# Performance work log

Measured on AMD Instinct MI355X. Metric: run time of the kernel, lower is better.

The kernel has to match this reference:

```python
import jax, jax.numpy as jnp
import numpy as np

L, B = 128, 64
IN_F, ACT_F, H = 512, 512, 1024
LSTM_IN = IN_F + ACT_F  # concat injection


def setup_inputs() -> dict:
    key = jax.random.key(0)
    ks = jax.random.split(key, 8)
    k = 1.0 / np.sqrt(H)  # torch LSTMCell init scale
    return {
        "input_feature": jax.random.normal(ks[0], (B, IN_F), dtype=jnp.float32),
        "action_features": jax.random.normal(ks[1], (L, B, ACT_F), dtype=jnp.float32),
        "hidden_state": jnp.zeros((B, H), dtype=jnp.float32),
        "state": jnp.zeros((B, H), dtype=jnp.float32),
        "W_ih": jax.random.uniform(ks[2], (4 * H, LSTM_IN), minval=-k, maxval=k, dtype=jnp.float32),
        "W_hh": jax.random.uniform(ks[3], (4 * H, H), minval=-k, maxval=k, dtype=jnp.float32),
        "b_ih": jax.random.uniform(ks[4], (4 * H,), minval=-k, maxval=k, dtype=jnp.float32),
        "b_hh": jax.random.uniform(ks[5], (4 * H,), minval=-k, maxval=k, dtype=jnp.float32),
    }


def reference(input_feature, action_features, hidden_state, state, W_ih, W_hh, b_ih, b_hh):
    # Per-timestep LSTMCell with concat injection of input_feature.
    # input_feature: [B, IN_F]; action_features: [L, B, ACT_F]
    def step(carry, a_t):
        h, c = carry
        x = jnp.concatenate([input_feature, a_t], axis=-1)  # inject_input (concat)
        gates = x @ W_ih.T + b_ih + h @ W_hh.T + b_hh  # [B, 4H]
        i, f, g, o = jnp.split(gates, 4, axis=-1)
        i = jax.nn.sigmoid(i)
        f = jax.nn.sigmoid(f)
        g = jnp.tanh(g)
        o = jax.nn.sigmoid(o)
        c1 = f * c + i * g
        h1 = o * jnp.tanh(c1)
        return (h1, c1), h1

    (h_n, c_n), hs = jax.lax.scan(step, (hidden_state, state), action_features)
    # hs: [L, B, H] stacked hidden states (PaddedSequenceWithMask.data)
    return hs, h_n, c_n
```

## Files before the change

kernel.cpp:

```cpp
#include <hip/hip_runtime.h>


#define LSTEPS 128
#define B 64
#define ACTF 512
#define H 1024
#define NB 128
#define HC 8
#define GSTR 37

typedef short s16x8 __attribute__((ext_vector_type(8)));
typedef short s16x4 __attribute__((ext_vector_type(4)));
typedef float f32x4 __attribute__((ext_vector_type(4)));
typedef unsigned short u16;
typedef unsigned long long u64;

__device__ __forceinline__ u16 f2bf(float f) {
  return __builtin_bit_cast(u16, (__bf16)f);
}
__device__ __forceinline__ float sigm(float x) { return 1.f / (1.f + __expf(-x)); }
__device__ __forceinline__ float tanh_fast(float x) { return 2.f / (1.f + __expf(-2.f * x)) - 1.f; }

__global__ void k_setup(const float* __restrict__ act, u16* __restrict__ actb,
                        const float* __restrict__ Wih, const float* __restrict__ Whh,
                        u16* __restrict__ wg,
                        const float* __restrict__ h0, u16* __restrict__ hbp,
                        const float* __restrict__ inf, const float* __restrict__ bih,
                        const float* __restrict__ bhh, float* __restrict__ pre0) {
  const int bb = blockIdx.x;
  const int tid = threadIdx.x;
  if (bb < 2048) {
    int id = bb * 256 + tid;
    const float4* s = (const float4*)act + (size_t)id * 2;
    float4 a = s[0], b = s[1];
    s16x8 o;
    o[0] = (short)f2bf(a.x); o[1] = (short)f2bf(a.y); o[2] = (short)f2bf(a.z); o[3] = (short)f2bf(a.w);
    o[4] = (short)f2bf(b.x); o[5] = (short)f2bf(b.y); o[6] = (short)f2bf(b.z); o[7] = (short)f2bf(b.w);
    int t = id >> 12, m = (id >> 6) & 63, ch = id & 63;
    ((s16x8*)actb)[t * 4096 + ch * 64 + m] = o;
  } else if (bb < 5120) {
    int idx = (bb - 2048) * 256 + tid;
    int bk = idx / 6144;
    int lin = idx - bk * 6144;
    int kt = lin >> 7, T = (lin >> 6) & 1, lane = lin & 63;
    int q = lane >> 4, r = lane & 15;
    int local = T * 16 + r;
    int j = (local >> 3) * 1024 + bk * 8 + (local & 7);
    int k = kt * 32 + q * 8;
    const float* src = (k < 512) ? (Wih + (size_t)j * 1024 + 512 + k)
                                 : (Whh + (size_t)j * 1024 + (k - 512));
    s16x8 o;
#pragma unroll
    for (int e = 0; e < 8; ++e) o[e] = (short)f2bf(src[e]);
    ((s16x8*)wg)[(size_t)bk * 6144 + lin] = o;
  } else if (bb < 5152) {
    int id = (bb - 5120) * 256 + tid;
    int blk2 = id >> 6, row = id & 63;
    const float* s = h0 + (size_t)row * H + blk2 * 8;
    s16x8 o;
#pragma unroll
    for (int e = 0; e < 8; ++e) o[e] = (short)f2bf(s[e]);
    o[0] = (short)((o[0] & ~1) | 1);
    ((s16x8*)(hbp + 65536))[blk2 * 64 + row] = o;
  } else if (bb < 5184) {
    int id = (bb - 5152) * 256 + tid;
    s16x8 p;
#pragma unroll
    for (int e = 0; e < 8; ++e) p[e] = 1;
    ((s16x8*)hbp)[id] = p;
  } else {
    int o = (bb - 5184) * 256 + tid;
    int bk = o >> 11;
    int rr = o & 2047;
    int b = rr >> 5;
    int local = rr & 31;
    int j = (local >> 3) * 1024 + bk * 8 + (local & 7);
    const float4* xa = (const float4*)(inf + (size_t)b * 512);
    const float4* wa = (const float4*)(Wih + (size_t)j * 1024);
    float s = 0.f;
#pragma unroll 4
    for (int k = 0; k < 128; ++k) {
      float4 x = xa[k], w = wa[k];
      s += x.x * w.x + x.y * w.y + x.z * w.z + x.w * w.w;
    }
    pre0[o] = s + bih[j] + bhh[j];
  }
}

#define AISS(dst, ptr) \
  asm volatile("global_load_dwordx4 %0, %1, off" : "=v"(dst) : "v"(ptr) : "memory");
#define HISS(dst, ptr) \
  asm volatile("global_load_dwordx4 %0, %1, off sc0 sc1" : "=v"(dst) : "v"(ptr) : "memory");
#define WAITV(N) { asm volatile("s_waitcnt vmcnt(" #N ")" ::: "memory"); \
                   __builtin_amdgcn_sched_barrier(0); }
#define LGKM0()  { asm volatile("s_waitcnt lgkmcnt(0)" ::: "memory"); }

__global__ void __launch_bounds__(256, 1) k_rnn(
    const u16* __restrict__ actb, const u16* __restrict__ wg,
    const float* __restrict__ pre0, const float* __restrict__ cinit,
    u16* __restrict__ hbp, unsigned* __restrict__ dump,
    float* __restrict__ out) {
  extern __shared__ char smem[];
  u16* wlds  = (u16*)smem;
  float* gl  = (float*)(smem + 98304);
  u16* hloc  = (u16*)(smem + 98304 + 37888);

  const int tid = threadIdx.x;
  const int bk = blockIdx.x;
  const int w = tid >> 6;
  const int lane = tid & 63;
  const int q = lane >> 4, r = lane & 15;
  const int n0 = bk * HC;
  const int prow = tid >> 1, pcg = (tid & 1) * 4;

  {
    const s16x8* src = (const s16x8*)wg + (size_t)bk * 6144;
    s16x8* dst = (s16x8*)wlds;
    for (int i = tid; i < 6144; i += 256) dst[i] = src[i];
  }

  float pr4[16], cr[4];
  if (tid < 128) {
#pragma unroll
    for (int g = 0; g < 4; ++g)
#pragma unroll
      for (int e = 0; e < 4; ++e)
        pr4[g * 4 + e] = pre0[bk * 2048 + prow * 32 + g * 8 + pcg + e];
#pragma unroll
    for (int e = 0; e < 4; ++e) cr[e] = cinit[prow * H + n0 + pcg + e];
  }
  if (tid < 64)
    *(s16x8*)(hloc + tid * 8) = ((const s16x8*)(hbp + 65536))[bk * 64 + tid];

  const bool ownw = (w == (bk >> 5));
  const int kown = (bk >> 2) & 7;
  const int qown = bk & 3;

  asm volatile("s_waitcnt vmcnt(0) lgkmcnt(0)" ::: "memory");
  __builtin_amdgcn_s_barrier();

  f32x4 hv_prev = {0.f, 0.f, 0.f, 0.f};

  for (int t = 0; t < LSTEPS; ++t) {
    s16x8 af[4][4];
    const u16* ab = actb + (size_t)t * 32768 + (w * 4) * 2048 + q * 512 + r * 8;
#define AISSG(KK) \
    AISS(af[KK][0], ab + (KK) * 2048);       AISS(af[KK][1], ab + (KK) * 2048 + 128); \
    AISS(af[KK][2], ab + (KK) * 2048 + 256); AISS(af[KK][3], ab + (KK) * 2048 + 384);
    AISSG(0) AISSG(1) AISSG(2) AISSG(3)
#undef AISSG

    if (t > 0) {
      if (w == 0) {
        s16x8 hu0 = *(const s16x8*)(hloc + lane * 8);
        u16* hp = hbp + (size_t)((t - 1) & 1) * 65536 + (size_t)bk * 512 + lane * 8;
        asm volatile("global_store_dwordx4 %0, %1, off sc0 sc1" :: "v"(hp), "v"(hu0) : "memory");
      } else {
        unsigned* dp = dump + (size_t)bk * 64 + lane;
        asm volatile("global_store_dword %0, %1, off" :: "v"(dp), "v"(0u) : "memory");
      }
      if (tid < 128) {
        float* op = out + (size_t)(t - 1) * 65536 + (size_t)prow * H + n0 + pcg;
        asm volatile("global_store_dwordx4 %0, %1, off" :: "v"(op), "v"(hv_prev) : "memory");
      } else {
        unsigned* dp = dump + (size_t)bk * 64 + lane;
        asm volatile("global_store_dword %0, %1, off" :: "v"(dp), "v"(0u) : "memory");
      }
    } else {
      unsigned* dp = dump + (size_t)bk * 64 + lane;
      asm volatile("global_store_dword %0, %1, off" :: "v"(dp), "v"(0u) : "memory");
      asm volatile("global_store_dword %0, %1, off" :: "v"(dp), "v"(0u) : "memory");
    }

    f32x4 acc[4][2];
#pragma unroll
    for (int mt = 0; mt < 4; ++mt) {
      f32x4 z = {0.f, 0.f, 0.f, 0.f};
      acc[mt][0] = z; acc[mt][1] = z;
    }

#define ACTCH(KK, VC) { \
      const s16x8* wb_ = (const s16x8*)wlds + (w * 4 + (KK)) * 128; \
      s16x8 b0_ = wb_[lane]; s16x8 b1_ = wb_[64 + lane]; \
      WAITV(VC) \
      acc[0][0] = __builtin_amdgcn_mfma_f32_16x16x32_bf16(af[KK][0], b0_, acc[0][0], 0, 0, 0); \
      acc[0][1] = __builtin_amdgcn_mfma_f32_16x16x32_bf16(af[KK][0], b1_, acc[0][1], 0, 0, 0); \
      acc[1][0] = __builtin_amdgcn_mfma_f32_16x16x32_bf16(af[KK][1], b0_, acc[1][0], 0, 0, 0); \
      acc[1][1] = __builtin_amdgcn_mfma_f32_16x16x32_bf16(af[KK][1], b1_, acc[1][1], 0, 0, 0); \
      acc[2][0] = __builtin_amdgcn_mfma_f32_16x16x32_bf16(af[KK][2], b0_, acc[2][0], 0, 0, 0); \
      acc[2][1] = __builtin_amdgcn_mfma_f32_16x16x32_bf16(af[KK][2], b1_, acc[2][1], 0, 0, 0); \
      acc[3][0] = __builtin_amdgcn_mfma_f32_16x16x32_bf16(af[KK][3], b0_, acc[3][0], 0, 0, 0); \
      acc[3][1] = __builtin_amdgcn_mfma_f32_16x16x32_bf16(af[KK][3], b1_, acc[3][1], 0, 0, 0); \
    }
    ACTCH(0, 14) ACTCH(1, 10) ACTCH(2, 6) ACTCH(3, 2)
#undef ACTCH

    const int wtag = ((t - 1) >> 1) & 1;
    const u16* hb2 = hbp + (size_t)((t - 1) & 1) * 65536 + ((w * 8) * 4 + q) * 512 + r * 8;
    s16x8 hu[8][4];
#define HISSG(I) \
    HISS(hu[I][0], hb2 + (I) * 2048)       HISS(hu[I][1], hb2 + (I) * 2048 + 128) \
    HISS(hu[I][2], hb2 + (I) * 2048 + 256) HISS(hu[I][3], hb2 + (I) * 2048 + 384)
    HISSG(0) HISSG(1) HISSG(2) HISSG(3) HISSG(4) HISSG(5) HISSG(6) HISSG(7)

#define SUBST(I) \
    if (ownw && (I) == kown && q == qown) { \
      hu[I][0] = *(const s16x8*)(hloc + (r +  0) * 8); \
      hu[I][1] = *(const s16x8*)(hloc + (r + 16) * 8); \
      hu[I][2] = *(const s16x8*)(hloc + (r + 32) * 8); \
      hu[I][3] = *(const s16x8*)(hloc + (r + 48) * 8); \
    }
#define CHECKOK(I, OK) { int bad_ = 0; \
      bad_ |= (hu[I][0][0] ^ wtag); bad_ |= (hu[I][1][0] ^ wtag); \
      bad_ |= (hu[I][2][0] ^ wtag); bad_ |= (hu[I][3][0] ^ wtag); \
      OK = ((bad_ & 1) == 0); }
#define DOMFMA(I) { \
      const s16x8* wb_ = (const s16x8*)wlds + (16 + w * 8 + (I)) * 128; \
      s16x8 b0_ = wb_[lane]; s16x8 b1_ = wb_[64 + lane]; \
      acc[0][0] = __builtin_amdgcn_mfma_f32_16x16x32_bf16(hu[I][0], b0_, acc[0][0], 0, 0, 0); \
      acc[0][1] = __builtin_amdgcn_mfma_f32_16x16x32_bf16(hu[I][0], b1_, acc[0][1], 0, 0, 0); \
      acc[1][0] = __builtin_amdgcn_mfma_f32_16x16x32_bf16(hu[I][1], b0_, acc[1][0], 0, 0, 0); \
      acc[1][1] = __builtin_amdgcn_mfma_f32_16x16x32_bf16(hu[I][1], b1_, acc[1][1], 0, 0, 0); \
      acc[2][0] = __builtin_amdgcn_mfma_f32_16x16x32_bf16(hu[I][2], b0_, acc[2][0], 0, 0, 0); \
      acc[2][1] = __builtin_amdgcn_mfma_f32_16x16x32_bf16(hu[I][2], b1_, acc[2][1], 0, 0, 0); \
      acc[3][0] = __builtin_amdgcn_mfma_f32_16x16x32_bf16(hu[I][3], b0_, acc[3][0], 0, 0, 0); \
      acc[3][1] = __builtin_amdgcn_mfma_f32_16x16x32_bf16(hu[I][3], b1_, acc[3][1], 0, 0, 0); \
    }

    unsigned stale = 0;
#define KSTEP(I, VC) { WAITV(VC) SUBST(I) int ok_; CHECKOK(I, ok_) \
      if (__all(ok_)) { DOMFMA(I) } else stale |= (1u << (I)); }
    KSTEP(0, 28) KSTEP(1, 24) KSTEP(2, 20) KSTEP(3, 16)
    KSTEP(4, 12) KSTEP(5, 8)  KSTEP(6, 4)  KSTEP(7, 0)
#undef KSTEP

    unsigned guard = 0;
    while (stale) {
      if (++guard > 256u) break;
      if (stale & 0x01u) { HISSG(0) } if (stale & 0x02u) { HISSG(1) }
      if (stale & 0x04u) { HISSG(2) } if (stale & 0x08u) { HISSG(3) }
      if (stale & 0x10u) { HISSG(4) } if (stale & 0x20u) { HISSG(5) }
      if (stale & 0x40u) { HISSG(6) } if (stale & 0x80u) { HISSG(7) }
      WAITV(0)
#define RETRY(I, M) if (stale & (M)) { SUBST(I) int ok_; CHECKOK(I, ok_) \
        if (__all(ok_)) { DOMFMA(I) stale &= ~(M); } }
      RETRY(0, 0x01u) RETRY(1, 0x02u) RETRY(2, 0x04u) RETRY(3, 0x08u)
      RETRY(4, 0x10u) RETRY(5, 0x20u) RETRY(6, 0x40u) RETRY(7, 0x80u)
#undef RETRY
    }
#undef HISSG
#undef SUBST
#undef CHECKOK
#undef DOMFMA

    {
      float* glw = gl + w * (64 * GSTR);
#pragma unroll
      for (int mt = 0; mt < 4; ++mt) {
        const int bb2 = mt * 16 + q * 4;
#pragma unroll
        for (int T = 0; T < 2; ++T) {
          const int lc = T * 16 + r;
#pragma unroll
          for (int e = 0; e < 4; ++e)
            glw[(bb2 + e) * GSTR + lc] = acc[mt][T][e];
        }
      }
    }
    LGKM0()
    __builtin_amdgcn_s_barrier();

    if (tid < 128) {
      const float* base = gl + prow * GSTR + pcg;
      f32x4 s0 = *(const f32x4*)(base);
      f32x4 s1 = *(const f32x4*)(base + 8);
      f32x4 s2 = *(const f32x4*)(base + 16);
      f32x4 s3 = *(const f32x4*)(base + 24);
#pragma unroll
      for (int ww = 1; ww < 4; ++ww) {
        const float* b2 = base + ww * (64 * GSTR);
        s0 += *(const f32x4*)(b2);
        s1 += *(const f32x4*)(b2 + 8);
        s2 += *(const f32x4*)(b2 + 16);
        s3 += *(const f32x4*)(b2 + 24);
      }
      float hv[4];
#pragma unroll
      for (int e = 0; e < 4; ++e) {
        float ig = sigm(s0[e] + pr4[e]);
        float fg = sigm(s1[e] + pr4[4 + e]);
        float gg = tanh_fast(s2[e] + pr4[8 + e]);
        float og = sigm(s3[e] + pr4[12 + e]);
        cr[e] = fg * cr[e] + ig * gg;
        hv[e] = og * tanh_fast(cr[e]);
        hv_prev[e] = hv[e];
      }
      const int ptag = (t >> 1) & 1;
      s16x4 hb;
      hb[0] = (short)f2bf(hv[0]); hb[1] = (short)f2bf(hv[1]);
      hb[2] = (short)f2bf(hv[2]); hb[3] = (short)f2bf(hv[3]);
      if (pcg == 0) hb[0] = (short)((hb[0] & ~1) | ptag);
      *(s16x4*)(hloc + prow * 8 + pcg) = hb;
    }
    LGKM0()
    __builtin_amdgcn_s_barrier();
  }

  if (tid < 128) {
    *(f32x4*)(out + (size_t)(LSTEPS - 1) * 65536 + (size_t)prow * H + n0 + pcg) = hv_prev;
    float* hn = out + (size_t)LSTEPS * 65536;
    float* cn = hn + 65536;
    *(f32x4*)(hn + (size_t)prow * H + n0 + pcg) = hv_prev;
    f32x4 cr4; cr4[0] = cr[0]; cr4[1] = cr[1]; cr4[2] = cr[2]; cr4[3] = cr[3];
    *(f32x4*)(cn + (size_t)prow * H + n0 + pcg) = cr4;
  }
}

extern "C" void kernel_launch(void* const* d_in, const int* in_sizes, int n_in,
                              void* d_out, int out_size, void* d_ws, size_t ws_size,
                              hipStream_t stream) {
  const float* inf = (const float*)d_in[0];
  const float* act = (const float*)d_in[1];
  const float* h0  = (const float*)d_in[2];
  const float* cst = (const float*)d_in[3];
  const float* Wih = (const float*)d_in[4];
  const float* Whh = (const float*)d_in[5];
  const float* bih = (const float*)d_in[6];
  const float* bhh = (const float*)d_in[7];
  float* out = (float*)d_out;

  char* ws = (char*)d_ws;
  u16* actb      = (u16*)ws;
  u16* wg        = (u16*)(ws + 8388608);
  float* pre0    = (float*)(ws + 20971520);
  u16* hbp       = (u16*)(ws + 22020096);
  unsigned* dump = (unsigned*)(ws + 23068672);

  hipLaunchKernelGGL(k_setup, dim3(6208), dim3(256), 0, stream,
                     act, actb, Wih, Whh, wg, h0, hbp,
                     inf, bih, bhh, pre0);

  hipFuncSetAttribute((const void*)k_rnn, hipFuncAttributeMaxDynamicSharedMemorySize, 137216);
  hipLaunchKernelGGL(k_rnn, dim3(NB), dim3(256), 137216, stream,
                     actb, wg, pre0, cst, hbp, dump, out);
}
```

Measured before the change: 889.6 us.

## Stage hidden state per XCC so blocks read h from local L2

Each block learns its XCC id and takes a rank through an atomic counter. The first 16 blocks on each XCC poll the global h buffer with uncached loads until the parity tag matches, then copy it into a staging buffer private to that XCC. Every block then invalidates its cache and reads h from the staging buffer with normal, L2-cacheable loads instead of system-coherent loads. The aim is to replace 128 blocks each pulling h across the fabric with one coherent fetch per XCC. The cost is an extra hop and a spin-wait on the critical path of every timestep, and it assumes each XCC hosts at least 16 blocks. Dump stores are also folded onto 16 slots.

```diff
diff --git a/kernel.cpp b/kernel.cpp
--- a/kernel.cpp
+++ b/kernel.cpp
@@ -25,6 +25,7 @@
                         const float* __restrict__ Wih, const float* __restrict__ Whh,
                         u16* __restrict__ wg,
                         const float* __restrict__ h0, u16* __restrict__ hbp,
+                        u16* __restrict__ stg, unsigned* __restrict__ xctr,
                         const float* __restrict__ inf, const float* __restrict__ bih,
                         const float* __restrict__ bhh, float* __restrict__ pre0) {
   const int bb = blockIdx.x;
@@ -68,8 +69,21 @@
 #pragma unroll
     for (int e = 0; e < 8; ++e) p[e] = 1;
     ((s16x8*)hbp)[id] = p;
+    if (bb == 5152 && tid < 8) xctr[tid] = 0u;
+  } else if (bb < 5312) {
+    int id = (bb - 5184) * 256 + tid;
+#pragma unroll
+    for (int e = 0; e < 4; ++e) {
+      int uu = id * 4 + e;
+      int par = (uu >> 13) & 1;
+      short lsb = (short)(1 ^ par);
+      s16x8 p;
+#pragma unroll
+      for (int k2 = 0; k2 < 8; ++k2) p[k2] = lsb;
+      ((s16x8*)stg)[uu] = p;
+    }
   } else {
-    int o = (bb - 5184) * 256 + tid;
+    int o = (bb - 5312) * 256 + tid;
     int bk = o >> 11;
     int rr = o & 2047;
     int b = rr >> 5;
@@ -89,6 +103,8 @@
 
 #define AISS(dst, ptr) \
   asm volatile("global_load_dwordx4 %0, %1, off" : "=v"(dst) : "v"(ptr) : "memory");
+#define PISS(dst, ptr) \
+  asm volatile("global_load_dwordx4 %0, %1, off" : "=v"(dst) : "v"(ptr) : "memory");
 #define HISS(dst, ptr) \
   asm volatile("global_load_dwordx4 %0, %1, off sc0 sc1" : "=v"(dst) : "v"(ptr) : "memory");
 #define WAITV(N) { asm volatile("s_waitcnt vmcnt(" #N ")" ::: "memory"); \
@@ -98,12 +114,14 @@
 __global__ void __launch_bounds__(256, 1) k_rnn(
     const u16* __restrict__ actb, const u16* __restrict__ wg,
     const float* __restrict__ pre0, const float* __restrict__ cinit,
-    u16* __restrict__ hbp, unsigned* __restrict__ dump,
+    u16* __restrict__ hbp, u16* __restrict__ stg,
+    unsigned* __restrict__ xctr, unsigned* __restrict__ dump,
     float* __restrict__ out) {
   extern __shared__ char smem[];
   u16* wlds  = (u16*)smem;
   float* gl  = (float*)(smem + 98304);
   u16* hloc  = (u16*)(smem + 98304 + 37888);
+  __shared__ int s_xcc, s_rank;
 
   const int tid = threadIdx.x;
   const int bk = blockIdx.x;
@@ -113,6 +131,14 @@
   const int n0 = bk * HC;
   const int prow = tid >> 1, pcg = (tid & 1) * 4;
 
+  if (tid == 0) {
+    unsigned xcc;
+    asm volatile("s_getreg_b32 %0, hwreg(HW_REG_XCC_ID)" : "=s"(xcc));
+    xcc &= 7u;
+    s_xcc = (int)xcc;
+    s_rank = (int)atomicAdd(&xctr[xcc], 1u);
+  }
+
   {
     const s16x8* src = (const s16x8*)wg + (size_t)bk * 6144;
     s16x8* dst = (s16x8*)wlds;
@@ -138,10 +164,16 @@
 
   asm volatile("s_waitcnt vmcnt(0) lgkmcnt(0)" ::: "memory");
   __builtin_amdgcn_s_barrier();
+  const int xcc = s_xcc;
+  const int rk = s_rank;
+  u16* stgx = stg + (size_t)xcc * 131072;
 
   f32x4 hv_prev = {0.f, 0.f, 0.f, 0.f};
 
   for (int t = 0; t < LSTEPS; ++t) {
+    const int par = (t - 1) & 1;
+    const int wtag = ((t - 1) >> 1) & 1;
+
     s16x8 af[4][4];
     const u16* ab = actb + (size_t)t * 32768 + (w * 4) * 2048 + q * 512 + r * 8;
 #define AISSG(KK) \
@@ -153,21 +185,21 @@
     if (t > 0) {
       if (w == 0) {
         s16x8 hu0 = *(const s16x8*)(hloc + lane * 8);
-        u16* hp = hbp + (size_t)((t - 1) & 1) * 65536 + (size_t)bk * 512 + lane * 8;
+        u16* hp = hbp + (size_t)par * 65536 + (size_t)bk * 512 + lane * 8;
         asm volatile("global_store_dwordx4 %0, %1, off sc0 sc1" :: "v"(hp), "v"(hu0) : "memory");
       } else {
-        unsigned* dp = dump + (size_t)bk * 64 + lane;
+        unsigned* dp = dump + ((bk & 15) * 64) + lane;
         asm volatile("global_store_dword %0, %1, off" :: "v"(dp), "v"(0u) : "memory");
       }
       if (tid < 128) {
         float* op = out + (size_t)(t - 1) * 65536 + (size_t)prow * H + n0 + pcg;
         asm volatile("global_store_dwordx4 %0, %1, off" :: "v"(op), "v"(hv_prev) : "memory");
       } else {
-        unsigned* dp = dump + (size_t)bk * 64 + lane;
+        unsigned* dp = dump + ((bk & 15) * 64) + lane;
         asm volatile("global_store_dword %0, %1, off" :: "v"(dp), "v"(0u) : "memory");
       }
     } else {
-      unsigned* dp = dump + (size_t)bk * 64 + lane;
+      unsigned* dp = dump + ((bk & 15) * 64) + lane;
       asm volatile("global_store_dword %0, %1, off" :: "v"(dp), "v"(0u) : "memory");
       asm volatile("global_store_dword %0, %1, off" :: "v"(dp), "v"(0u) : "memory");
     }
@@ -195,13 +227,31 @@
     ACTCH(0, 14) ACTCH(1, 10) ACTCH(2, 6) ACTCH(3, 2)
 #undef ACTCH
 
-    const int wtag = ((t - 1) >> 1) & 1;
-    const u16* hb2 = hbp + (size_t)((t - 1) & 1) * 65536 + ((w * 8) * 4 + q) * 512 + r * 8;
+    if (rk < 16) {
+      const u16* sp0 = hbp + (size_t)par * 65536 + ((size_t)rk * 512 + tid) * 8;
+      const u16* sp1 = sp0 + 2048;
+      u16* dd0 = stgx + (size_t)par * 65536 + ((size_t)rk * 512 + tid) * 8;
+      u16* dd1 = dd0 + 2048;
+      s16x8 v0, v1;
+      unsigned g = 0;
+      for (;;) {
+        HISS(v0, sp0) HISS(v1, sp1) WAITV(0)
+        int ok = (((v0[0] ^ wtag) | (v1[0] ^ wtag)) & 1) == 0;
+        if (__all(ok)) break;
+        if (++g > 2048u) break;
+      }
+      *(s16x8*)dd0 = v0;
+      *(s16x8*)dd1 = v1;
+    }
+    WAITV(0)
+    asm volatile("buffer_inv sc0" ::: "memory");
+
+    const u16* hb2 = stgx + (size_t)par * 65536 + ((w * 8) * 4 + q) * 512 + r * 8;
     s16x8 hu[8][4];
-#define HISSG(I) \
-    HISS(hu[I][0], hb2 + (I) * 2048)       HISS(hu[I][1], hb2 + (I) * 2048 + 128) \
-    HISS(hu[I][2], hb2 + (I) * 2048 + 256) HISS(hu[I][3], hb2 + (I) * 2048 + 384)
-    HISSG(0) HISSG(1) HISSG(2) HISSG(3) HISSG(4) HISSG(5) HISSG(6) HISSG(7)
+#define PISSG(I) \
+    PISS(hu[I][0], hb2 + (I) * 2048)       PISS(hu[I][1], hb2 + (I) * 2048 + 128) \
+    PISS(hu[I][2], hb2 + (I) * 2048 + 256) PISS(hu[I][3], hb2 + (I) * 2048 + 384)
+    PISSG(0) PISSG(1) PISSG(2) PISSG(3) PISSG(4) PISSG(5) PISSG(6) PISSG(7)
 
 #define SUBST(I) \
     if (ownw && (I) == kown && q == qown) { \
@@ -236,11 +286,12 @@
 
     unsigned guard = 0;
     while (stale) {
-      if (++guard > 256u) break;
-      if (stale & 0x01u) { HISSG(0) } if (stale & 0x02u) { HISSG(1) }
-      if (stale & 0x04u) { HISSG(2) } if (stale & 0x08u) { HISSG(3) }
-      if (stale & 0x10u) { HISSG(4) } if (stale & 0x20u) { HISSG(5) }
-      if (stale & 0x40u) { HISSG(6) } if (stale & 0x80u) { HISSG(7) }
+      if (++guard > 512u) break;
+      asm volatile("buffer_inv sc0" ::: "memory");
+      if (stale & 0x01u) { PISSG(0) } if (stale & 0x02u) { PISSG(1) }
+      if (stale & 0x04u) { PISSG(2) } if (stale & 0x08u) { PISSG(3) }
+      if (stale & 0x10u) { PISSG(4) } if (stale & 0x20u) { PISSG(5) }
+      if (stale & 0x40u) { PISSG(6) } if (stale & 0x80u) { PISSG(7) }
       WAITV(0)
 #define RETRY(I, M) if (stale & (M)) { SUBST(I) int ok_; CHECKOK(I, ok_) \
         if (__all(ok_)) { DOMFMA(I) stale &= ~(M); } }
@@ -248,7 +299,7 @@
       RETRY(4, 0x10u) RETRY(5, 0x20u) RETRY(6, 0x40u) RETRY(7, 0x80u)
 #undef RETRY
     }
-#undef HISSG
+#undef PISSG
 #undef SUBST
 #undef CHECKOK
 #undef DOMFMA
@@ -334,13 +385,15 @@
   u16* wg        = (u16*)(ws + 8388608);
   float* pre0    = (float*)(ws + 20971520);
   u16* hbp       = (u16*)(ws + 22020096);
-  unsigned* dump = (unsigned*)(ws + 23068672);
-
-  hipLaunchKernelGGL(k_setup, dim3(6208), dim3(256), 0, stream,
-                     act, actb, Wih, Whh, wg, h0, hbp,
+  u16* stg       = (u16*)(ws + 22282240);
+  unsigned* dump = (unsigned*)(ws + 24379392);
+  unsigned* xctr = (unsigned*)(ws + 24383488);
+
+  hipLaunchKernelGGL(k_setup, dim3(6336), dim3(256), 0, stream,
+                     act, actb, Wih, Whh, wg, h0, hbp, stg, xctr,
                      inf, bih, bhh, pre0);
 
   hipFuncSetAttribute((const void*)k_rnn, hipFuncAttributeMaxDynamicSharedMemorySize, 137216);
   hipLaunchKernelGGL(k_rnn, dim3(NB), dim3(256), 137216, stream,
-                     actb, wg, pre0, cst, hbp, dump, out);
+                     actb, wg, pre0, cst, hbp, stg, xctr, dump, out);
 }
```

New measurement: 1.277 ms. 1.44x slower.
